# Optimization experiments

Hardware: AMD Instinct MI355X
Metric: run time of the kernel (lower is better)

Reference implementation:

```python
import jax, jax.numpy as jnp
import numpy as np

EPS = 1e-5


def tbn(x, g, b):
    # TensorBatchNorm2d(121): normalize each of the 11x11 tensor entries over (B, C, H, W)
    mu = x.mean(axis=(0, 1, 2, 3), keepdims=True)
    var = ((x - mu) ** 2).mean(axis=(0, 1, 2, 3), keepdims=True)
    return (x - mu) * jax.lax.rsqrt(var + EPS) * g + b


def prelu(x, a):
    return jnp.where(x >= 0, x, a * x)


def tconv1x1(x, U, V):
    # x: [B,1,H,W,m,n]; U: [p,m]; V: [q,n] -> y[...,p,q] = U @ X @ V^T
    return jnp.einsum('bchwmn,pm,qn->bchwpq', x, U, V)


def tconv3x3(x, U, V):
    # x: [B,1,H,W,m,n]; U,V: [3,3,p,m] / [3,3,q,n]; pad=1, stride=1
    H, W = x.shape[2], x.shape[3]
    xp = jnp.pad(x, ((0, 0), (0, 0), (1, 1), (1, 1), (0, 0), (0, 0)))
    y = jnp.zeros(x.shape[:4] + (U.shape[2], V.shape[2]), x.dtype)
    for i in range(3):
        for j in range(3):
            y = y + jnp.einsum('bchwmn,pm,qn->bchwpq', xp[:, :, i:i + H, j:j + W], U[i, j], V[i, j])
    return y


def forward(x, f0_U, f0_V, f0_g, f0_b, f0_a, s_U, s_V, s_g, s_b,
            blk_U1, blk_V1, blk_g1, blk_b1, blk_a1,
            blk_U2, blk_V2, blk_g2, blk_b2, blk_a2,
            blk_U3, blk_V3, blk_g3, blk_b3, head_W):
    # view(-1,8,16,16,32,32).permute(0,1,4,5,2,3) -> [B,8,32,32,16,16]
    x = x.reshape(-1, 8, 16, 16, 32, 32).transpose(0, 1, 4, 5, 2, 3)
    B, H, W = x.shape[0], 32, 32
    # f0: 3x3 tensorized conv, 8 channels -> 1, tensor 16x16 -> 11x11
    xp = jnp.pad(x, ((0, 0), (0, 0), (1, 1), (1, 1), (0, 0), (0, 0)))
    y = jnp.zeros((B, H, W, 11, 11), x.dtype)
    for i in range(3):
        for j in range(3):
            y = y + jnp.einsum('bchwmn,cpm,cqn->bhwpq', xp[:, :, i:i + H, j:j + W], f0_U[:, i, j], f0_V[:, i, j])
    h = prelu(tbn(y[:, None], f0_g, f0_b), f0_a)  # [B,1,32,32,11,11]
    for k in range(4):  # four residual bottleneck blocks with 1x1 shortcut
        idn = tbn(tconv1x1(h, s_U[k], s_V[k]), s_g[k], s_b[k])
        z = prelu(tbn(tconv1x1(h, blk_U1[k], blk_V1[k]), blk_g1[k], blk_b1[k]), blk_a1[k])
        z = prelu(tbn(tconv3x3(z, blk_U2[k], blk_V2[k]), blk_g2[k], blk_b2[k]), blk_a2[k])
        z = tbn(tconv1x1(z, blk_U3[k], blk_V3[k]), blk_g3[k], blk_b3[k])
        h = z + idn
    # fcn_head: 1x1, out_type=0 -> fully contract the [11,11] tensor per class
    return jnp.einsum('bchwmn,omn->bohw', h, head_W)  # [B,21,32,32]


def setup_inputs():
    ks = jax.random.split(jax.random.key(0), 26)
    r = lambda i, s: jax.random.normal(ks[i], s, dtype=jnp.float32)
    return {
        'x': r(0, (64, 8, 16, 16, 32, 32)),
        'f0_U': r(1, (8, 3, 3, 11, 16)) * 0.1,
        'f0_V': r(2, (8, 3, 3, 11, 16)) * 0.1,
        'f0_g': r(3, (11, 11)), 'f0_b': r(4, (11, 11)),
        'f0_a': jnp.float32(0.25),
        's_U': r(5, (4, 11, 11)) * 0.3, 's_V': r(6, (4, 11, 11)) * 0.3,
        's_g': r(7, (4, 11, 11)), 's_b': r(8, (4, 11, 11)),
        'blk_U1': r(9, (4, 11, 11)) * 0.3, 'blk_V1': r(10, (4, 11, 11)) * 0.3,
        'blk_g1': r(11, (4, 11, 11)), 'blk_b1': r(12, (4, 11, 11)),
        'blk_a1': jax.random.uniform(ks[13], (4,), dtype=jnp.float32),
        'blk_U2': r(14, (4, 3, 3, 11, 11)) * 0.2, 'blk_V2': r(15, (4, 3, 3, 11, 11)) * 0.2,
        'blk_g2': r(16, (4, 11, 11)), 'blk_b2': r(17, (4, 11, 11)),
        'blk_a2': jax.random.uniform(ks[18], (4,), dtype=jnp.float32),
        'blk_U3': r(19, (4, 11, 11)) * 0.3, 'blk_V3': r(20, (4, 11, 11)) * 0.3,
        'blk_g3': r(21, (4, 11, 11)), 'blk_b3': r(22, (4, 11, 11)),
        'head_W': r(23, (21, 11, 11)) * 0.1,
    }


def reference(x, f0_U, f0_V, f0_g, f0_b, f0_a, s_U, s_V, s_g, s_b,
              blk_U1, blk_V1, blk_g1, blk_b1, blk_a1,
              blk_U2, blk_V2, blk_g2, blk_b2, blk_a2,
              blk_U3, blk_V3, blk_g3, blk_b3, head_W):
    return forward(x, f0_U, f0_V, f0_g, f0_b, f0_a, s_U, s_V, s_g, s_b,
                   blk_U1, blk_V1, blk_g1, blk_b1, blk_a1,
                   blk_U2, blk_V2, blk_g2, blk_b2, blk_a2,
                   blk_U3, blk_V3, blk_g3, blk_b3, head_W)
```

## Files before the change

### kernel.cpp

```cpp
#include <hip/hip_runtime.h>

#define NPOS 65536
#define NE   121
#define NP   6
#define NPP  4

__device__ __forceinline__ void gload_lds16(const float* g, float* l) {
  __builtin_amdgcn_global_load_lds(
      (const __attribute__((address_space(1))) void*)g,
      (__attribute__((address_space(3))) void*)l, 16, 0, 0);
}

__global__ __launch_bounds__(256, 1)
void f0_kernel(const float* __restrict__ x, const float* __restrict__ U,
               const float* __restrict__ V, float* __restrict__ y,
               float* __restrict__ psum, float* __restrict__ psq) {
  __shared__ float Xb[16384];
  __shared__ float su[1152];
  __shared__ float sv[1728];

  int bid = blockIdx.x;
  int wg  = (bid & 7) * 512 + (bid >> 3);
  int ph  = wg & 1;
  int row = wg >> 1;
  int b = row >> 5, h = row & 31;
  int P0 = ph * 5;
  int t = threadIdx.x;
  int s = t >> 5, w = t & 31;

  int hlo = (h == 0) ? 0 : h - 1;
  int hhi = (h == 31) ? 31 : h + 1;
  int nh = hhi - hlo + 1;
  int nslab = 8 * nh;

  float Y[NP][11];
#pragma unroll
  for (int p = 0; p < NP; ++p)
#pragma unroll
    for (int q = 0; q < 11; ++q) Y[p][q] = 0.f;

  auto stageUV = [&](int c) {
    for (int idx = t; idx < 1152; idx += 256) {
      int tap = idx >> 7, r = idx & 127;
      int m = r >> 3, pr = r & 7;
      su[idx] = (pr < 6) ? U[(c * 9 + tap) * 176 + (P0 + pr) * 16 + m] : 0.f;
    }
    for (int idx = t; idx < 1728; idx += 256) {
      int tap = idx / 192, r = idx - tap * 192;
      int n = r / 12, q = r - n * 12;
      sv[idx] = (q < 11) ? V[(c * 9 + tap) * 176 + q * 16 + n] : 0.f;
    }
  };

  auto issueX = [&](int k) {
    int c = k / nh, hi = hlo + k % nh;
    const float* base = x + ((size_t)(b * 8 + c) << 18) + hi * 32;
    float* buf = &Xb[(k & 1) * 8192];
    int wv = t >> 6, ln = t & 63;
#pragma unroll
    for (int kk = 0; kk < 8; ++kk) {
      int chunk = wv * 8 + kk;
      int mn = chunk * 8 + (ln >> 3);
      gload_lds16(base + (size_t)mn * 1024 + (ln & 7) * 4, buf + chunk * 256);
    }
  };

  stageUV(0);
  issueX(0);

  for (int k = 0; k < nslab; ++k) {
    asm volatile("s_waitcnt vmcnt(0)" ::: "memory");
    __syncthreads();
    if (k + 1 < nslab) issueX(k + 1);

    const float* Xt = &Xb[(k & 1) * 8192];
    int c = k / nh, hi = hlo + k % nh;
    int tapbase = (hi - h + 1) * 3;
#pragma unroll
    for (int j = 0; j < 3; ++j) {
      int wj = w + j - 1;
      if ((unsigned)wj < 32u) {
        int tap = tapbase + j;
        const float* suT = &su[tap * 128];
        const float* svT = &sv[tap * 192];
        float A0[6], A1[6];
#pragma unroll
        for (int p = 0; p < 6; ++p) { A0[p] = 0.f; A1[p] = 0.f; }
#pragma unroll
        for (int m = 0; m < 16; ++m) {
          float x0 = Xt[(m * 16 + 2 * s) * 32 + wj];
          float x1 = Xt[(m * 16 + 2 * s + 1) * 32 + wj];
          float4 u0 = *(const float4*)&suT[m * 8];
          float2 u1 = *(const float2*)&suT[m * 8 + 4];
          A0[0] += u0.x * x0; A1[0] += u0.x * x1;
          A0[1] += u0.y * x0; A1[1] += u0.y * x1;
          A0[2] += u0.z * x0; A1[2] += u0.z * x1;
          A0[3] += u0.w * x0; A1[3] += u0.w * x1;
          A0[4] += u1.x * x0; A1[4] += u1.x * x1;
          A0[5] += u1.y * x0; A1[5] += u1.y * x1;
        }
#pragma unroll
        for (int nn = 0; nn < 2; ++nn) {
          const float* vb = &svT[(2 * s + nn) * 12];
          float4 v0 = *(const float4*)&vb[0];
          float4 v1 = *(const float4*)&vb[4];
          float4 v2 = *(const float4*)&vb[8];
          float vq[11] = { v0.x, v0.y, v0.z, v0.w,
                           v1.x, v1.y, v1.z, v1.w,
                           v2.x, v2.y, v2.z };
          const float* Ax = nn ? A1 : A0;
#pragma unroll
          for (int p = 0; p < 6; ++p)
#pragma unroll
            for (int q = 0; q < 11; ++q)
              Y[p][q] += Ax[p] * vq[q];
        }
      }
    }
    if (k + 1 < nslab && (k % nh) == nh - 1) {
      __syncthreads();
      stageUV(c + 1);
    }
  }

  int posb = ((b << 5) + h) << 5;
#pragma unroll
  for (int p = 0; p < NP; ++p) {
    __syncthreads();
#pragma unroll
    for (int q = 0; q < 11; ++q) Xb[t * 11 + q] = Y[p][q];
    __syncthreads();
    for (int rep = 0; rep < 2; ++rep) {
      int idx = rep * 256 + t;
      if (idx < 352) {
        int qq = idx >> 5, w2 = idx & 31;
        float v = 0.f;
#pragma unroll
        for (int s2 = 0; s2 < 8; ++s2) v += Xb[(s2 * 32 + w2) * 11 + qq];
        int e = (P0 + p) * 11 + qq;
        y[(size_t)e * NPOS + posb + w2] = v;
        float sm = v, sq = v * v;
#pragma unroll
        for (int d = 16; d > 0; d >>= 1) {
          sm += __shfl_down(sm, d, 32);
          sq += __shfl_down(sq, d, 32);
        }
        if (w2 == 0) {
          psum[(size_t)e * 2048 + row] = sm;
          psq [(size_t)e * 2048 + row] = sq;
        }
      }
    }
  }
}

__global__ __launch_bounds__(256)
void f0_stats_final(const float* __restrict__ psum, const float* __restrict__ psq,
                    const float* __restrict__ g, const float* __restrict__ bb,
                    float* __restrict__ sc, float* __restrict__ sh) {
  int e = blockIdx.x, t = threadIdx.x;
  float s = 0.f, s2 = 0.f;
  for (int i = t; i < 2048; i += 256) {
    s  += psum[(size_t)e * 2048 + i];
    s2 += psq [(size_t)e * 2048 + i];
  }
#pragma unroll
  for (int o = 32; o > 0; o >>= 1) {
    s  += __shfl_down(s, o);
    s2 += __shfl_down(s2, o);
  }
  __shared__ float ls[8];
  int wid = t >> 6;
  if ((t & 63) == 0) { ls[wid] = s; ls[4 + wid] = s2; }
  __syncthreads();
  if (t == 0) {
    float ss  = ls[0] + ls[1] + ls[2] + ls[3];
    float ss2 = ls[4] + ls[5] + ls[6] + ls[7];
    float mu  = ss  * (1.f / 65536.f);
    float var = ss2 * (1.f / 65536.f) - mu * mu;
    float sca = g[e] * rsqrtf(var + 1e-5f);
    sc[e] = sca;
    sh[e] = bb[e] - mu * sca;
  }
}

__global__ __launch_bounds__(256)
void stats_kernel(const float* __restrict__ raw, const float* __restrict__ g,
                  const float* __restrict__ bb, float* __restrict__ sc,
                  float* __restrict__ sh) {
  int e = blockIdx.x;
  const float4* p = (const float4*)(raw + (size_t)e * NPOS);
  int t = threadIdx.x;
  float s = 0.f, s2 = 0.f;
  for (int i = t; i < 16384; i += 256) {
    float4 v = p[i];
    s  += v.x + v.y + v.z + v.w;
    s2 += v.x * v.x + v.y * v.y + v.z * v.z + v.w * v.w;
  }
#pragma unroll
  for (int o = 32; o > 0; o >>= 1) {
    s  += __shfl_down(s, o);
    s2 += __shfl_down(s2, o);
  }
  __shared__ float ls[8];
  int wid = t >> 6;
  if ((t & 63) == 0) { ls[wid] = s; ls[4 + wid] = s2; }
  __syncthreads();
  if (t == 0) {
    float ss  = ls[0] + ls[1] + ls[2] + ls[3];
    float ss2 = ls[4] + ls[5] + ls[6] + ls[7];
    float mu  = ss  * (1.f / 65536.f);
    float var = ss2 * (1.f / 65536.f) - mu * mu;
    float sca = g[e] * rsqrtf(var + 1e-5f);
    sc[e] = sca;
    sh[e] = bb[e] - mu * sca;
  }
}

__global__ __launch_bounds__(256)
void stats_dual(const float* __restrict__ rawA, const float* __restrict__ gA,
                const float* __restrict__ bA, float* __restrict__ scA,
                float* __restrict__ shA,
                const float* __restrict__ rawB, const float* __restrict__ gB,
                const float* __restrict__ bB, float* __restrict__ scB,
                float* __restrict__ shB) {
  int sel = blockIdx.x >= 121;
  int e = blockIdx.x - (sel ? 121 : 0);
  const float* raw = sel ? rawB : rawA;
  const float* g   = sel ? gB : gA;
  const float* bb  = sel ? bB : bA;
  float* sc = sel ? scB : scA;
  float* sh = sel ? shB : shA;

  const float4* p = (const float4*)(raw + (size_t)e * NPOS);
  int t = threadIdx.x;
  float s = 0.f, s2 = 0.f;
  for (int i = t; i < 16384; i += 256) {
    float4 v = p[i];
    s  += v.x + v.y + v.z + v.w;
    s2 += v.x * v.x + v.y * v.y + v.z * v.z + v.w * v.w;
  }
#pragma unroll
  for (int o = 32; o > 0; o >>= 1) {
    s  += __shfl_down(s, o);
    s2 += __shfl_down(s2, o);
  }
  __shared__ float ls[8];
  int wid = t >> 6;
  if ((t & 63) == 0) { ls[wid] = s; ls[4 + wid] = s2; }
  __syncthreads();
  if (t == 0) {
    float ss  = ls[0] + ls[1] + ls[2] + ls[3];
    float ss2 = ls[4] + ls[5] + ls[6] + ls[7];
    float mu  = ss  * (1.f / 65536.f);
    float var = ss2 * (1.f / 65536.f) - mu * mu;
    float sca = g[e] * rsqrtf(var + 1e-5f);
    sc[e] = sca;
    sh[e] = bb[e] - mu * sca;
  }
}

template<bool HASB, bool PRELU>
__global__ __launch_bounds__(256, 2)
void conv1x1_dual(const float* __restrict__ rA, const float* __restrict__ scA,
                  const float* __restrict__ shA,
                  const float* __restrict__ rB, const float* __restrict__ scB,
                  const float* __restrict__ shB,
                  const float* __restrict__ alpha_ptr, int alpha_idx,
                  const float* __restrict__ U1, const float* __restrict__ V1,
                  float* __restrict__ out1,
                  const float* __restrict__ U2, const float* __restrict__ V2,
                  float* __restrict__ out2) {
  __shared__ float su1[NPP * 11], su2[NPP * 11], sv1[121], sv2[121];
  __shared__ float sa[242], sb[242];
  int bid = blockIdx.x;
  int wg  = (bid & 7) * 96 + (bid >> 3);
  int part = wg % 3, posblk = wg / 3;
  int P0 = part * 4;
  int pmax = (part == 2) ? 3 : 4;
  int t = threadIdx.x;
  if (t < 121) {
    sv1[t] = V1[t]; sv2[t] = V2[t];
    sa[t] = scA[t]; sb[t] = shA[t];
    if (HASB) { sa[121 + t] = scB[t]; sb[121 + t] = shB[t]; }
  }
  if (t < NPP * 11) {
    int pr = t / 11, mm = t - pr * 11;
    int srow = P0 + pr; if (srow > 10) srow = 10;
    su1[t] = U1[srow * 11 + mm];
    su2[t] = U2[srow * 11 + mm];
  }
  __syncthreads();
  float alpha = 0.f;
  if (PRELU) alpha = alpha_ptr[alpha_idx];
  size_t pos = (size_t)posblk * 256 + t;

  float T1[NPP][11], T2[NPP][11];
#pragma unroll
  for (int p = 0; p < NPP; ++p)
#pragma unroll
    for (int n = 0; n < 11; ++n) { T1[p][n] = 0.f; T2[p][n] = 0.f; }

#pragma unroll 2
  for (int m = 0; m < 11; ++m) {
    float Xr[11];
#pragma unroll
    for (int n = 0; n < 11; ++n) {
      int e = m * 11 + n;
      float v = sa[e] * rA[(size_t)e * NPOS + pos] + sb[e];
      if (HASB) v += sa[121 + e] * rB[(size_t)e * NPOS + pos] + sb[121 + e];
      if (PRELU) v = v >= 0.f ? v : alpha * v;
      Xr[n] = v;
    }
#pragma unroll
    for (int p = 0; p < NPP; ++p) {
      float u1 = su1[p * 11 + m];
      float u2 = su2[p * 11 + m];
#pragma unroll
      for (int n = 0; n < 11; ++n) {
        T1[p][n] += u1 * Xr[n];
        T2[p][n] += u2 * Xr[n];
      }
    }
  }
#pragma unroll
  for (int q = 0; q < 11; ++q) {
    float Yc1[NPP], Yc2[NPP];
#pragma unroll
    for (int p = 0; p < NPP; ++p) { Yc1[p] = 0.f; Yc2[p] = 0.f; }
#pragma unroll
    for (int n = 0; n < 11; ++n) {
      float v1 = sv1[q * 11 + n];
      float v2 = sv2[q * 11 + n];
#pragma unroll
      for (int p = 0; p < NPP; ++p) {
        Yc1[p] += T1[p][n] * v1;
        Yc2[p] += T2[p][n] * v2;
      }
    }
    for (int p = 0; p < pmax; ++p) {
      out1[(size_t)((P0 + p) * 11 + q) * NPOS + pos] = Yc1[p];
      out2[(size_t)((P0 + p) * 11 + q) * NPOS + pos] = Yc2[p];
    }
  }
}

template<bool HASB, bool PRELU>
__global__ __launch_bounds__(256, 2)
void conv1x1_kernel(const float* __restrict__ rA, const float* __restrict__ scA,
                    const float* __restrict__ shA,
                    const float* __restrict__ rB, const float* __restrict__ scB,
                    const float* __restrict__ shB,
                    const float* __restrict__ alpha_ptr, int alpha_idx,
                    const float* __restrict__ U, const float* __restrict__ V,
                    float* __restrict__ out) {
  __shared__ float su[NP * 11], sv[121], sa[242], sb[242];
  int bid = blockIdx.x;
  int wg  = (bid & 7) * 64 + (bid >> 3);
  int ph = wg & 1, posblk = wg >> 1;
  int P0 = ph * 5;
  int t = threadIdx.x;
  if (t < 121) {
    sv[t] = V[t];
    sa[t] = scA[t]; sb[t] = shA[t];
    if (HASB) { sa[121 + t] = scB[t]; sb[121 + t] = shB[t]; }
  }
  if (t < NP * 11) su[t] = U[P0 * 11 + t];
  __syncthreads();
  float alpha = 0.f;
  if (PRELU) alpha = alpha_ptr[alpha_idx];
  size_t pos = (size_t)posblk * 256 + t;

  float T[NP][11];
#pragma unroll
  for (int p = 0; p < NP; ++p)
#pragma unroll
    for (int n = 0; n < 11; ++n) T[p][n] = 0.f;

#pragma unroll 2
  for (int m = 0; m < 11; ++m) {
    float Xr[11];
#pragma unroll
    for (int n = 0; n < 11; ++n) {
      int e = m * 11 + n;
      float v = sa[e] * rA[(size_t)e * NPOS + pos] + sb[e];
      if (HASB) v += sa[121 + e] * rB[(size_t)e * NPOS + pos] + sb[121 + e];
      if (PRELU) v = v >= 0.f ? v : alpha * v;
      Xr[n] = v;
    }
#pragma unroll
    for (int p = 0; p < NP; ++p) {
      float u = su[p * 11 + m];
#pragma unroll
      for (int n = 0; n < 11; ++n) T[p][n] += u * Xr[n];
    }
  }
#pragma unroll
  for (int q = 0; q < 11; ++q) {
    float Yc[NP];
#pragma unroll
    for (int p = 0; p < NP; ++p) Yc[p] = 0.f;
#pragma unroll
    for (int n = 0; n < 11; ++n) {
      float v = sv[q * 11 + n];
#pragma unroll
      for (int p = 0; p < NP; ++p) Yc[p] += T[p][n] * v;
    }
#pragma unroll
    for (int p = 0; p < NP; ++p)
      out[(size_t)((P0 + p) * 11 + q) * NPOS + pos] = Yc[p];
  }
}

template<int N0, int NW>
__device__ __forceinline__ void c3_chunk(const float* __restrict__ rA,
    const float* __restrict__ sa, const float* __restrict__ sh,
    const float* __restrict__ su, const float* __restrict__ sv,
    float alpha, int npos, float (&Y)[NP][11]) {
  float T[NP][NW];
#pragma unroll
  for (int p = 0; p < NP; ++p)
#pragma unroll
    for (int k = 0; k < NW; ++k) T[p][k] = 0.f;
#pragma unroll 2
  for (int m = 0; m < 11; ++m) {
    float Xr[NW];
#pragma unroll
    for (int k = 0; k < NW; ++k) {
      int e = m * 11 + N0 + k;
      float v = sa[e] * rA[(size_t)e * NPOS + npos] + sh[e];
      Xr[k] = v >= 0.f ? v : alpha * v;
    }
#pragma unroll
    for (int p = 0; p < NP; ++p) {
      float u = su[p * 11 + m];
#pragma unroll
      for (int k = 0; k < NW; ++k) T[p][k] += u * Xr[k];
    }
  }
#pragma unroll
  for (int k = 0; k < NW; ++k) {
#pragma unroll
    for (int q = 0; q < 11; ++q) {
      float v = sv[q * 11 + N0 + k];
#pragma unroll
      for (int p = 0; p < NP; ++p) Y[p][q] += T[p][k] * v;
    }
  }
}

__global__ __launch_bounds__(256, 2)
void conv3x3_kernel(const float* __restrict__ rA, const float* __restrict__ scA,
                    const float* __restrict__ shA,
                    const float* __restrict__ alpha_ptr, int alpha_idx,
                    const float* __restrict__ U, const float* __restrict__ V,
                    float* __restrict__ out) {
  __shared__ float su[9 * NP * 11], sv[1089], sa[121], sh[121];
  int bid = blockIdx.x;
  int wg  = (bid & 7) * 64 + (bid >> 3);
  int ph = wg & 1, posblk = wg >> 1;
  int P0 = ph * 5;
  int t = threadIdx.x;
  for (int idx = t; idx < 9 * NP * 11; idx += 256) {
    int ij = idx / (NP * 11), r = idx - ij * (NP * 11);
    su[idx] = U[ij * 121 + P0 * 11 + r];
  }
  for (int idx = t; idx < 1089; idx += 256) sv[idx] = V[idx];
  if (t < 121) { sa[t] = scA[t]; sh[t] = shA[t]; }
  __syncthreads();
  float alpha = alpha_ptr[alpha_idx];
  int pos = posblk * 256 + t;
  int b = pos >> 10, h = (pos >> 5) & 31, w = pos & 31;

  float Y[NP][11];
#pragma unroll
  for (int p = 0; p < NP; ++p)
#pragma unroll
    for (int q = 0; q < 11; ++q) Y[p][q] = 0.f;

  for (int ij = 0; ij < 9; ++ij) {
    int i = ij / 3, j = ij - 3 * (ij / 3);
    int hi = h + i - 1, wj = w + j - 1;
    if ((unsigned)hi >= 32u || (unsigned)wj >= 32u) continue;
    int npos = ((b << 5) + hi) * 32 + wj;
    const float* suij = &su[ij * NP * 11];
    const float* svij = &sv[ij * 121];
    c3_chunk<0, 4>(rA, sa, sh, suij, svij, alpha, npos, Y);
    c3_chunk<4, 4>(rA, sa, sh, suij, svij, alpha, npos, Y);
    c3_chunk<8, 3>(rA, sa, sh, suij, svij, alpha, npos, Y);
  }
#pragma unroll
  for (int p = 0; p < NP; ++p)
#pragma unroll
    for (int q = 0; q < 11; ++q)
      out[(size_t)((P0 + p) * 11 + q) * NPOS + pos] = Y[p][q];
}

__global__ __launch_bounds__(256, 2)
void head_kernel(const float* __restrict__ rA, const float* __restrict__ scA,
                 const float* __restrict__ shA,
                 const float* __restrict__ rB, const float* __restrict__ scB,
                 const float* __restrict__ shB,
                 const float* __restrict__ W, float* __restrict__ out) {
  __shared__ float sw[21 * 121], sa[242], sh[242];
  int t = threadIdx.x;
  for (int idx = t; idx < 2541; idx += 256) sw[idx] = W[idx];
  if (t < 121) {
    sa[t] = scA[t]; sh[t] = shA[t];
    sa[121 + t] = scB[t]; sh[121 + t] = shB[t];
  }
  __syncthreads();
  size_t pos = (size_t)blockIdx.x * 256 + t;
  int b = (int)(pos >> 10), hw = (int)(pos & 1023);
  float acc[21];
#pragma unroll
  for (int o = 0; o < 21; ++o) acc[o] = 0.f;
  for (int e = 0; e < 121; ++e) {
    float v = sa[e] * rA[(size_t)e * NPOS + pos] + sh[e] +
              sa[121 + e] * rB[(size_t)e * NPOS + pos] + sh[121 + e];
#pragma unroll
    for (int o = 0; o < 21; ++o) acc[o] += v * sw[o * 121 + e];
  }
#pragma unroll
  for (int o = 0; o < 21; ++o)
    out[(size_t)(b * 21 + o) * 1024 + hw] = acc[o];
}

extern "C" void kernel_launch(void* const* d_in, const int* in_sizes, int n_in,
                              void* d_out, int out_size, void* d_ws, size_t ws_size,
                              hipStream_t stream) {
  (void)in_sizes; (void)n_in; (void)out_size; (void)ws_size;
  const float* x     = (const float*)d_in[0];
  const float* f0_U  = (const float*)d_in[1];
  const float* f0_V  = (const float*)d_in[2];
  const float* f0_g  = (const float*)d_in[3];
  const float* f0_b  = (const float*)d_in[4];
  const float* f0_a  = (const float*)d_in[5];
  const float* s_U   = (const float*)d_in[6];
  const float* s_V   = (const float*)d_in[7];
  const float* s_g   = (const float*)d_in[8];
  const float* s_b   = (const float*)d_in[9];
  const float* bU1   = (const float*)d_in[10];
  const float* bV1   = (const float*)d_in[11];
  const float* bg1   = (const float*)d_in[12];
  const float* bb1   = (const float*)d_in[13];
  const float* ba1   = (const float*)d_in[14];
  const float* bU2   = (const float*)d_in[15];
  const float* bV2   = (const float*)d_in[16];
  const float* bg2   = (const float*)d_in[17];
  const float* bb2   = (const float*)d_in[18];
  const float* ba2   = (const float*)d_in[19];
  const float* bU3   = (const float*)d_in[20];
  const float* bV3   = (const float*)d_in[21];
  const float* bg3   = (const float*)d_in[22];
  const float* bb3   = (const float*)d_in[23];
  const float* headW = (const float*)d_in[24];

  float* ws = (float*)d_ws;
  const size_t BUF = (size_t)NE * NPOS;
  float* B[4]  = { ws, ws + BUF, ws + 2 * BUF, ws + 3 * BUF };
  float* st    = ws + 4 * BUF;
  float* psum  = st + 17 * 242;
  float* psq   = psum + 121 * 2048;

  auto SCp = [&](int op) { return st + op * 242; };
  auto SHp = [&](int op) { return st + op * 242 + 121; };

  f0_kernel<<<4096, 256, 0, stream>>>(x, f0_U, f0_V, B[0], psum, psq);
  f0_stats_final<<<121, 256, 0, stream>>>(psum, psq, f0_g, f0_b, SCp(0), SHp(0));

  const int bufs[4][4] = { {1,2,3,0}, {2,3,0,1}, {3,0,1,2}, {0,1,2,3} };

  const float* hA   = B[0];  const float* hAsc = SCp(0); const float* hAsh = SHp(0);
  const float* hB   = nullptr; const float* hBsc = nullptr; const float* hBsh = nullptr;

  for (int k = 0; k < 4; ++k) {
    float* idn = B[bufs[k][0]];
    float* z1  = B[bufs[k][1]];
    float* z2  = B[bufs[k][2]];
    float* z3  = B[bufs[k][3]];
    int op_idn = 1 + k * 4, op_z1 = 2 + k * 4, op_z2 = 3 + k * 4, op_z3 = 4 + k * 4;

    if (k == 0) {
      conv1x1_dual<false, true><<<768, 256, 0, stream>>>(
          hA, hAsc, hAsh, nullptr, nullptr, nullptr, f0_a, 0,
          s_U + k * 121, s_V + k * 121, idn,
          bU1 + k * 121, bV1 + k * 121, z1);
    } else {
      conv1x1_dual<true, false><<<768, 256, 0, stream>>>(
          hA, hAsc, hAsh, hB, hBsc, hBsh, nullptr, 0,
          s_U + k * 121, s_V + k * 121, idn,
          bU1 + k * 121, bV1 + k * 121, z1);
    }
    stats_dual<<<242, 256, 0, stream>>>(
        idn, s_g + k * 121, s_b + k * 121, SCp(op_idn), SHp(op_idn),
        z1,  bg1 + k * 121, bb1 + k * 121, SCp(op_z1),  SHp(op_z1));

    conv3x3_kernel<<<512, 256, 0, stream>>>(
        z1, SCp(op_z1), SHp(op_z1), ba1, k,
        bU2 + k * 1089, bV2 + k * 1089, z2);
    stats_kernel<<<121, 256, 0, stream>>>(z2, bg2 + k * 121, bb2 + k * 121,
                                          SCp(op_z2), SHp(op_z2));

    conv1x1_kernel<false, true><<<512, 256, 0, stream>>>(
        z2, SCp(op_z2), SHp(op_z2), nullptr, nullptr, nullptr, ba2, k,
        bU3 + k * 121, bV3 + k * 121, z3);
    stats_kernel<<<121, 256, 0, stream>>>(z3, bg3 + k * 121, bb3 + k * 121,
                                          SCp(op_z3), SHp(op_z3));

    hA = z3;  hAsc = SCp(op_z3);  hAsh = SHp(op_z3);
    hB = idn; hBsc = SCp(op_idn); hBsh = SHp(op_idn);
  }

  head_kernel<<<256, 256, 0, stream>>>(hA, hAsc, hAsh, hB, hBsc, hBsh,
                                       headW, (float*)d_out);
}
```

Before: 1.778 ms.

## Load X slab into registers once and shift tap partials via lane shuffles

```diff
diff --git a/kernel.cpp b/kernel.cpp
--- a/kernel.cpp
+++ b/kernel.cpp
@@ -16,7 +16,7 @@
                const float* __restrict__ V, float* __restrict__ y,
                float* __restrict__ psum, float* __restrict__ psq) {
   __shared__ float Xb[16384];
-  __shared__ float su[1152];
+  __shared__ float su[864];
   __shared__ float sv[1728];
 
   int bid = blockIdx.x;
@@ -27,6 +27,7 @@
   int P0 = ph * 5;
   int t = threadIdx.x;
   int s = t >> 5, w = t & 31;
+  int lane = t & 63;
 
   int hlo = (h == 0) ? 0 : h - 1;
   int hhi = (h == 31) ? 31 : h + 1;
@@ -40,10 +41,9 @@
     for (int q = 0; q < 11; ++q) Y[p][q] = 0.f;
 
   auto stageUV = [&](int c) {
-    for (int idx = t; idx < 1152; idx += 256) {
-      int tap = idx >> 7, r = idx & 127;
-      int m = r >> 3, pr = r & 7;
-      su[idx] = (pr < 6) ? U[(c * 9 + tap) * 176 + (P0 + pr) * 16 + m] : 0.f;
+    for (int idx = t; idx < 864; idx += 256) {
+      int tap = idx / 96, r = idx - tap * 96;
+      su[idx] = U[(c * 9 + tap) * 176 + P0 * 16 + r];
     }
     for (int idx = t; idx < 1728; idx += 256) {
       int tap = idx / 192, r = idx - tap * 192;
@@ -76,47 +76,68 @@
     const float* Xt = &Xb[(k & 1) * 8192];
     int c = k / nh, hi = hlo + k % nh;
     int tapbase = (hi - h + 1) * 3;
+
+    float xr0[16], xr1[16];
+#pragma unroll
+    for (int m = 0; m < 16; ++m) {
+      xr0[m] = Xt[(m * 16 + 2 * s) * 32 + w];
+      xr1[m] = Xt[(m * 16 + 2 * s + 1) * 32 + w];
+    }
+
+    float A[3][6][2];
 #pragma unroll
     for (int j = 0; j < 3; ++j) {
-      int wj = w + j - 1;
-      if ((unsigned)wj < 32u) {
-        int tap = tapbase + j;
-        const float* suT = &su[tap * 128];
-        const float* svT = &sv[tap * 192];
-        float A0[6], A1[6];
-#pragma unroll
-        for (int p = 0; p < 6; ++p) { A0[p] = 0.f; A1[p] = 0.f; }
+      const float* suT = &su[(tapbase + j) * 96];
+#pragma unroll
+      for (int p = 0; p < 6; ++p) {
+        float4 u0 = *(const float4*)&suT[p * 16 + 0];
+        float4 u1 = *(const float4*)&suT[p * 16 + 4];
+        float4 u2 = *(const float4*)&suT[p * 16 + 8];
+        float4 u3 = *(const float4*)&suT[p * 16 + 12];
+        float uu[16] = { u0.x, u0.y, u0.z, u0.w, u1.x, u1.y, u1.z, u1.w,
+                         u2.x, u2.y, u2.z, u2.w, u3.x, u3.y, u3.z, u3.w };
+        float a0 = 0.f, a1 = 0.f;
 #pragma unroll
         for (int m = 0; m < 16; ++m) {
-          float x0 = Xt[(m * 16 + 2 * s) * 32 + wj];
-          float x1 = Xt[(m * 16 + 2 * s + 1) * 32 + wj];
-          float4 u0 = *(const float4*)&suT[m * 8];
-          float2 u1 = *(const float2*)&suT[m * 8 + 4];
-          A0[0] += u0.x * x0; A1[0] += u0.x * x1;
-          A0[1] += u0.y * x0; A1[1] += u0.y * x1;
-          A0[2] += u0.z * x0; A1[2] += u0.z * x1;
-          A0[3] += u0.w * x0; A1[3] += u0.w * x1;
-          A0[4] += u1.x * x0; A1[4] += u1.x * x1;
-          A0[5] += u1.y * x0; A1[5] += u1.y * x1;
+          a0 += uu[m] * xr0[m];
+          a1 += uu[m] * xr1[m];
         }
-#pragma unroll
-        for (int nn = 0; nn < 2; ++nn) {
-          const float* vb = &svT[(2 * s + nn) * 12];
-          float4 v0 = *(const float4*)&vb[0];
-          float4 v1 = *(const float4*)&vb[4];
-          float4 v2 = *(const float4*)&vb[8];
-          float vq[11] = { v0.x, v0.y, v0.z, v0.w,
-                           v1.x, v1.y, v1.z, v1.w,
-                           v2.x, v2.y, v2.z };
-          const float* Ax = nn ? A1 : A0;
-#pragma unroll
-          for (int p = 0; p < 6; ++p)
-#pragma unroll
-            for (int q = 0; q < 11; ++q)
-              Y[p][q] += Ax[p] * vq[q];
+        A[j][p][0] = a0; A[j][p][1] = a1;
+      }
+    }
+
+#pragma unroll
+    for (int p = 0; p < 6; ++p)
+#pragma unroll
+      for (int nn = 0; nn < 2; ++nn) {
+        float a0 = __shfl(A[0][p][nn], lane - 1, 64);
+        float a2 = __shfl(A[2][p][nn], lane + 1, 64);
+        A[0][p][nn] = (w == 0)  ? 0.f : a0;
+        A[2][p][nn] = (w == 31) ? 0.f : a2;
+      }
+
+#pragma unroll
+    for (int j = 0; j < 3; ++j) {
+      int tap = tapbase + j;
+#pragma unroll
+      for (int nn = 0; nn < 2; ++nn) {
+        const float* vb = &sv[tap * 192 + (2 * s + nn) * 12];
+        float4 v0 = *(const float4*)&vb[0];
+        float4 v1 = *(const float4*)&vb[4];
+        float4 v2 = *(const float4*)&vb[8];
+        float vq[11] = { v0.x, v0.y, v0.z, v0.w,
+                         v1.x, v1.y, v1.z, v1.w,
+                         v2.x, v2.y, v2.z };
+#pragma unroll
+        for (int p = 0; p < 6; ++p) {
+          float a = A[j][p][nn];
+#pragma unroll
+          for (int q = 0; q < 11; ++q)
+            Y[p][q] += a * vq[q];
         }
       }
     }
+
     if (k + 1 < nslab && (k % nh) == nh - 1) {
       __syncthreads();
       stageUV(c + 1);
```

Result: slower. 2.531 ms (+42.4%).

## Split BN stats reduction into quarter blocks and finalize in consumer kernels

Applied to the files above, without the earlier changes.

```diff
diff --git a/kernel.cpp b/kernel.cpp
--- a/kernel.cpp
+++ b/kernel.cpp
@@ -9,6 +9,19 @@
   __builtin_amdgcn_global_load_lds(
       (const __attribute__((address_space(1))) void*)g,
       (__attribute__((address_space(3))) void*)l, 16, 0, 0);
+}
+
+__device__ __forceinline__ void fin_from_part(int e, const float* __restrict__ pp,
+                                              const float* __restrict__ g,
+                                              const float* __restrict__ bb,
+                                              float& sc, float& sh) {
+  float s  = pp[e * 4] + pp[e * 4 + 1] + pp[e * 4 + 2] + pp[e * 4 + 3];
+  float s2 = pp[484 + e * 4] + pp[484 + e * 4 + 1] +
+             pp[484 + e * 4 + 2] + pp[484 + e * 4 + 3];
+  float mu  = s  * (1.f / 65536.f);
+  float var = s2 * (1.f / 65536.f) - mu * mu;
+  sc = g[e] * rsqrtf(var + 1e-5f);
+  sh = bb[e] - mu * sc;
 }
 
 __global__ __launch_bounds__(256, 1)
@@ -185,14 +198,13 @@
 }
 
 __global__ __launch_bounds__(256)
-void stats_kernel(const float* __restrict__ raw, const float* __restrict__ g,
-                  const float* __restrict__ bb, float* __restrict__ sc,
-                  float* __restrict__ sh) {
-  int e = blockIdx.x;
-  const float4* p = (const float4*)(raw + (size_t)e * NPOS);
+void stats_partial(const float* __restrict__ raw, float* __restrict__ part) {
+  int blk = blockIdx.x;
+  int e = blk >> 2, qt = blk & 3;
+  const float4* p = (const float4*)(raw + (size_t)e * NPOS) + qt * 4096;
   int t = threadIdx.x;
   float s = 0.f, s2 = 0.f;
-  for (int i = t; i < 16384; i += 256) {
+  for (int i = t; i < 4096; i += 256) {
     float4 v = p[i];
     s  += v.x + v.y + v.z + v.w;
     s2 += v.x * v.x + v.y * v.y + v.z * v.z + v.w * v.w;
@@ -207,35 +219,24 @@
   if ((t & 63) == 0) { ls[wid] = s; ls[4 + wid] = s2; }
   __syncthreads();
   if (t == 0) {
-    float ss  = ls[0] + ls[1] + ls[2] + ls[3];
-    float ss2 = ls[4] + ls[5] + ls[6] + ls[7];
-    float mu  = ss  * (1.f / 65536.f);
-    float var = ss2 * (1.f / 65536.f) - mu * mu;
-    float sca = g[e] * rsqrtf(var + 1e-5f);
-    sc[e] = sca;
-    sh[e] = bb[e] - mu * sca;
+    part[blk]       = ls[0] + ls[1] + ls[2] + ls[3];
+    part[484 + blk] = ls[4] + ls[5] + ls[6] + ls[7];
   }
 }
 
 __global__ __launch_bounds__(256)
-void stats_dual(const float* __restrict__ rawA, const float* __restrict__ gA,
-                const float* __restrict__ bA, float* __restrict__ scA,
-                float* __restrict__ shA,
-                const float* __restrict__ rawB, const float* __restrict__ gB,
-                const float* __restrict__ bB, float* __restrict__ scB,
-                float* __restrict__ shB) {
-  int sel = blockIdx.x >= 121;
-  int e = blockIdx.x - (sel ? 121 : 0);
+void stats_partial_dual(const float* __restrict__ rawA, float* __restrict__ partA,
+                        const float* __restrict__ rawB, float* __restrict__ partB) {
+  int blk = blockIdx.x;
+  int sel = blk >= 484;
+  int lblk = sel ? blk - 484 : blk;
   const float* raw = sel ? rawB : rawA;
-  const float* g   = sel ? gB : gA;
-  const float* bb  = sel ? bB : bA;
-  float* sc = sel ? scB : scA;
-  float* sh = sel ? shB : shA;
-
-  const float4* p = (const float4*)(raw + (size_t)e * NPOS);
+  float* part = sel ? partB : partA;
+  int e = lblk >> 2, qt = lblk & 3;
+  const float4* p = (const float4*)(raw + (size_t)e * NPOS) + qt * 4096;
   int t = threadIdx.x;
   float s = 0.f, s2 = 0.f;
-  for (int i = t; i < 16384; i += 256) {
+  for (int i = t; i < 4096; i += 256) {
     float4 v = p[i];
     s  += v.x + v.y + v.z + v.w;
     s2 += v.x * v.x + v.y * v.y + v.z * v.z + v.w * v.w;
@@ -250,22 +251,20 @@
   if ((t & 63) == 0) { ls[wid] = s; ls[4 + wid] = s2; }
   __syncthreads();
   if (t == 0) {
-    float ss  = ls[0] + ls[1] + ls[2] + ls[3];
-    float ss2 = ls[4] + ls[5] + ls[6] + ls[7];
-    float mu  = ss  * (1.f / 65536.f);
-    float var = ss2 * (1.f / 65536.f) - mu * mu;
-    float sca = g[e] * rsqrtf(var + 1e-5f);
-    sc[e] = sca;
-    sh[e] = bb[e] - mu * sca;
-  }
-}
-
-template<bool HASB, bool PRELU>
+    part[lblk]       = ls[0] + ls[1] + ls[2] + ls[3];
+    part[484 + lblk] = ls[4] + ls[5] + ls[6] + ls[7];
+  }
+}
+
+template<bool HASB, bool PRELU, bool FINA, bool FINB>
 __global__ __launch_bounds__(256, 2)
-void conv1x1_dual(const float* __restrict__ rA, const float* __restrict__ scA,
-                  const float* __restrict__ shA,
-                  const float* __restrict__ rB, const float* __restrict__ scB,
-                  const float* __restrict__ shB,
+void conv1x1_dual(const float* __restrict__ rA,
+                  const float* __restrict__ scA, const float* __restrict__ shA,
+                  const float* __restrict__ pA, const float* __restrict__ gA,
+                  const float* __restrict__ bA,
+                  const float* __restrict__ rB,
+                  const float* __restrict__ pB, const float* __restrict__ gB,
+                  const float* __restrict__ bB,
                   const float* __restrict__ alpha_ptr, int alpha_idx,
                   const float* __restrict__ U1, const float* __restrict__ V1,
                   float* __restrict__ out1,
@@ -281,8 +280,11 @@
   int t = threadIdx.x;
   if (t < 121) {
     sv1[t] = V1[t]; sv2[t] = V2[t];
-    sa[t] = scA[t]; sb[t] = shA[t];
-    if (HASB) { sa[121 + t] = scB[t]; sb[121 + t] = shB[t]; }
+    if (FINA) fin_from_part(t, pA, gA, bA, sa[t], sb[t]);
+    else      { sa[t] = scA[t]; sb[t] = shA[t]; }
+    if (HASB) {
+      if (FINB) fin_from_part(t, pB, gB, bB, sa[121 + t], sb[121 + t]);
+    }
   }
   if (t < NPP * 11) {
     int pr = t / 11, mm = t - pr * 11;
@@ -345,12 +347,11 @@
   }
 }
 
-template<bool HASB, bool PRELU>
+template<bool PRELU>
 __global__ __launch_bounds__(256, 2)
-void conv1x1_kernel(const float* __restrict__ rA, const float* __restrict__ scA,
-                    const float* __restrict__ shA,
-                    const float* __restrict__ rB, const float* __restrict__ scB,
-                    const float* __restrict__ shB,
+void conv1x1_kernel(const float* __restrict__ rA,
+                    const float* __restrict__ pA, const float* __restrict__ gA,
+                    const float* __restrict__ bA,
                     const float* __restrict__ alpha_ptr, int alpha_idx,
                     const float* __restrict__ U, const float* __restrict__ V,
                     float* __restrict__ out) {
@@ -362,8 +363,7 @@
   int t = threadIdx.x;
   if (t < 121) {
     sv[t] = V[t];
-    sa[t] = scA[t]; sb[t] = shA[t];
-    if (HASB) { sa[121 + t] = scB[t]; sb[121 + t] = shB[t]; }
+    fin_from_part(t, pA, gA, bA, sa[t], sb[t]);
   }
   if (t < NP * 11) su[t] = U[P0 * 11 + t];
   __syncthreads();
@@ -384,7 +384,6 @@
     for (int n = 0; n < 11; ++n) {
       int e = m * 11 + n;
       float v = sa[e] * rA[(size_t)e * NPOS + pos] + sb[e];
-      if (HASB) v += sa[121 + e] * rB[(size_t)e * NPOS + pos] + sb[121 + e];
       if (PRELU) v = v >= 0.f ? v : alpha * v;
       Xr[n] = v;
     }
@@ -450,8 +449,9 @@
 }
 
 __global__ __launch_bounds__(256, 2)
-void conv3x3_kernel(const float* __restrict__ rA, const float* __restrict__ scA,
-                    const float* __restrict__ shA,
+void conv3x3_kernel(const float* __restrict__ rA,
+                    const float* __restrict__ pA, const float* __restrict__ gA,
+                    const float* __restrict__ bA,
                     const float* __restrict__ alpha_ptr, int alpha_idx,
                     const float* __restrict__ U, const float* __restrict__ V,
                     float* __restrict__ out) {
@@ -466,7 +466,7 @@
     su[idx] = U[ij * 121 + P0 * 11 + r];
   }
   for (int idx = t; idx < 1089; idx += 256) sv[idx] = V[idx];
-  if (t < 121) { sa[t] = scA[t]; sh[t] = shA[t]; }
+  if (t < 121) fin_from_part(t, pA, gA, bA, sa[t], sh[t]);
   __syncthreads();
   float alpha = alpha_ptr[alpha_idx];
   int pos = posblk * 256 + t;
@@ -497,17 +497,19 @@
 }
 
 __global__ __launch_bounds__(256, 2)
-void head_kernel(const float* __restrict__ rA, const float* __restrict__ scA,
-                 const float* __restrict__ shA,
-                 const float* __restrict__ rB, const float* __restrict__ scB,
-                 const float* __restrict__ shB,
+void head_kernel(const float* __restrict__ rA,
+                 const float* __restrict__ pA, const float* __restrict__ gA,
+                 const float* __restrict__ bA,
+                 const float* __restrict__ rB,
+                 const float* __restrict__ pB, const float* __restrict__ gB,
+                 const float* __restrict__ bB,
                  const float* __restrict__ W, float* __restrict__ out) {
   __shared__ float sw[21 * 121], sa[242], sh[242];
   int t = threadIdx.x;
   for (int idx = t; idx < 2541; idx += 256) sw[idx] = W[idx];
   if (t < 121) {
-    sa[t] = scA[t]; sh[t] = shA[t];
-    sa[121 + t] = scB[t]; sh[121 + t] = shB[t];
+    fin_from_part(t, pA, gA, bA, sa[t], sh[t]);
+    fin_from_part(t, pB, gB, bB, sa[121 + t], sh[121 + t]);
   }
   __syncthreads();
   size_t pos = (size_t)blockIdx.x * 256 + t;
@@ -560,58 +562,60 @@
   const size_t BUF = (size_t)NE * NPOS;
   float* B[4]  = { ws, ws + BUF, ws + 2 * BUF, ws + 3 * BUF };
   float* st    = ws + 4 * BUF;
-  float* psum  = st + 17 * 242;
+  float* psum  = st + 242;
   float* psq   = psum + 121 * 2048;
-
-  auto SCp = [&](int op) { return st + op * 242; };
-  auto SHp = [&](int op) { return st + op * 242 + 121; };
+  float* pb0   = psq + 121 * 2048;
+  float* pb1   = pb0 + 968;
+  float* pb2   = pb1 + 968;
+  float* pb3   = pb2 + 968;
 
   f0_kernel<<<4096, 256, 0, stream>>>(x, f0_U, f0_V, B[0], psum, psq);
-  f0_stats_final<<<121, 256, 0, stream>>>(psum, psq, f0_g, f0_b, SCp(0), SHp(0));
+  f0_stats_final<<<121, 256, 0, stream>>>(psum, psq, f0_g, f0_b, st, st + 121);
 
   const int bufs[4][4] = { {1,2,3,0}, {2,3,0,1}, {3,0,1,2}, {0,1,2,3} };
 
-  const float* hA   = B[0];  const float* hAsc = SCp(0); const float* hAsh = SHp(0);
-  const float* hB   = nullptr; const float* hBsc = nullptr; const float* hBsh = nullptr;
+  const float* hA = B[0];
+  const float* hB = nullptr;
 
   for (int k = 0; k < 4; ++k) {
     float* idn = B[bufs[k][0]];
     float* z1  = B[bufs[k][1]];
     float* z2  = B[bufs[k][2]];
     float* z3  = B[bufs[k][3]];
-    int op_idn = 1 + k * 4, op_z1 = 2 + k * 4, op_z2 = 3 + k * 4, op_z3 = 4 + k * 4;
 
     if (k == 0) {
-      conv1x1_dual<false, true><<<768, 256, 0, stream>>>(
-          hA, hAsc, hAsh, nullptr, nullptr, nullptr, f0_a, 0,
+      conv1x1_dual<false, true, false, false><<<768, 256, 0, stream>>>(
+          hA, st, st + 121, nullptr, nullptr, nullptr,
+          nullptr, nullptr, nullptr, nullptr,
+          f0_a, 0,
           s_U + k * 121, s_V + k * 121, idn,
           bU1 + k * 121, bV1 + k * 121, z1);
     } else {
-      conv1x1_dual<true, false><<<768, 256, 0, stream>>>(
-          hA, hAsc, hAsh, hB, hBsc, hBsh, nullptr, 0,
+      conv1x1_dual<true, false, true, true><<<768, 256, 0, stream>>>(
+          hA, nullptr, nullptr, pb3, bg3 + (k - 1) * 121, bb3 + (k - 1) * 121,
+          hB, pb0, s_g + (k - 1) * 121, s_b + (k - 1) * 121,
+          nullptr, 0,
           s_U + k * 121, s_V + k * 121, idn,
           bU1 + k * 121, bV1 + k * 121, z1);
     }
-    stats_dual<<<242, 256, 0, stream>>>(
-        idn, s_g + k * 121, s_b + k * 121, SCp(op_idn), SHp(op_idn),
-        z1,  bg1 + k * 121, bb1 + k * 121, SCp(op_z1),  SHp(op_z1));
+    stats_partial_dual<<<968, 256, 0, stream>>>(idn, pb0, z1, pb1);
 
     conv3x3_kernel<<<512, 256, 0, stream>>>(
-        z1, SCp(op_z1), SHp(op_z1), ba1, k,
+        z1, pb1, bg1 + k * 121, bb1 + k * 121, ba1, k,
         bU2 + k * 1089, bV2 + k * 1089, z2);
-    stats_kernel<<<121, 256, 0, stream>>>(z2, bg2 + k * 121, bb2 + k * 121,
-                                          SCp(op_z2), SHp(op_z2));
-
-    conv1x1_kernel<false, true><<<512, 256, 0, stream>>>(
-        z2, SCp(op_z2), SHp(op_z2), nullptr, nullptr, nullptr, ba2, k,
+    stats_partial<<<484, 256, 0, stream>>>(z2, pb2);
+
+    conv1x1_kernel<true><<<512, 256, 0, stream>>>(
+        z2, pb2, bg2 + k * 121, bb2 + k * 121, ba2, k,
         bU3 + k * 121, bV3 + k * 121, z3);
-    stats_kernel<<<121, 256, 0, stream>>>(z3, bg3 + k * 121, bb3 + k * 121,
-                                          SCp(op_z3), SHp(op_z3));
-
-    hA = z3;  hAsc = SCp(op_z3);  hAsh = SHp(op_z3);
-    hB = idn; hBsc = SCp(op_idn); hBsh = SHp(op_idn);
-  }
-
-  head_kernel<<<256, 256, 0, stream>>>(hA, hAsc, hAsh, hB, hBsc, hBsh,
-                                       headW, (float*)d_out);
-}
+    stats_partial<<<484, 256, 0, stream>>>(z3, pb3);
+
+    hA = z3;
+    hB = idn;
+  }
+
+  head_kernel<<<256, 256, 0, stream>>>(
+      hA, pb3, bg3 + 3 * 121, bb3 + 3 * 121,
+      hB, pb0, s_g + 3 * 121, s_b + 3 * 121,
+      headW, (float*)d_out);
+}
```

After: 1.640 ms (median of 2 runs). -7.8%, faster.
